# Kernel tuning notes

Hardware: AMD Instinct MI355X
Metric: run time of the kernel (lower is better)

The kernel has to match this reference:

```python
import jax, jax.numpy as jnp
import numpy as np

B, S, D_IN, D_K, D_OUT = 8, 2048, 1024, 64, 64

def setup_inputs() -> dict:
    key = jax.random.key(0)
    k1, k2, k3, k4 = jax.random.split(key, 4)
    sc = 1.0 / np.sqrt(D_IN)
    return {
        "X": jax.random.normal(k1, (B, S, D_IN), dtype=jnp.float32),
        "Wq": jax.random.normal(k2, (D_IN, D_K), dtype=jnp.float32) * sc,
        "Wk": jax.random.normal(k3, (D_IN, D_K), dtype=jnp.float32) * sc,
        "Wv": jax.random.normal(k4, (D_IN, D_OUT), dtype=jnp.float32) * sc,
    }

def reference(X, Wq, Wk, Wv):
    # projections (no bias)
    Q = jnp.einsum('bsd,dk->bsk', X, Wq)   # [B,S,d_k]
    K = jnp.einsum('bsd,dk->bsk', X, Wk)   # [B,S,d_k]
    V = jnp.einsum('bsd,dv->bsv', X, Wv)   # [B,S,d_out]
    d_k = Q.shape[-1]
    S_mat = jnp.einsum('bqk,bsk->bqs', Q, K) / jnp.sqrt(jnp.float32(d_k))
    # causal mask: positions j > i get -inf
    causal = jnp.tril(jnp.ones((X.shape[1], X.shape[1]), dtype=bool))
    S_mat = jnp.where(causal[None, :, :], S_mat, -jnp.inf)
    A = jax.nn.softmax(S_mat, axis=-1)
    return jnp.einsum('bqs,bsv->bqv', A, V)
```

## Files before the change

### kernel.cpp

```cpp
#include <hip/hip_runtime.h>
#include <hip/hip_bf16.h>
#include <cstdint>
#include <cstddef>

#define BATCH 8
#define SEQ   2048
#define DIN   1024

typedef float f32x4 __attribute__((ext_vector_type(4)));
typedef float f32x8 __attribute__((ext_vector_type(8)));
typedef __bf16 bf16x4 __attribute__((ext_vector_type(4)));
typedef __bf16 bf16x8 __attribute__((ext_vector_type(8)));
typedef unsigned short ushort8_t __attribute__((ext_vector_type(8)));

__device__ __forceinline__ unsigned short bfu(float f) {
  __bf16 h = (__bf16)f;
  return __builtin_bit_cast(unsigned short, h);
}

__device__ __forceinline__ bf16x8 cvt8pair(float4 a, float4 b) {
  f32x8 v;
  v[0] = a.x; v[1] = a.y; v[2] = a.z; v[3] = a.w;
  v[4] = b.x; v[5] = b.y; v[6] = b.z; v[7] = b.w;
  return __builtin_convertvector(v, bf16x8);
}

__global__ void pack_w(const float* __restrict__ Wq, const float* __restrict__ Wk,
                       const float* __restrict__ Wv, unsigned short* __restrict__ Wp) {
  const int t = blockIdx.x * blockDim.x + threadIdx.x;
  const int lane = t & 63;
  const int grp = t >> 6;
  const int ks = grp & 31;
  const int nt = grp >> 5;
  const int n = nt * 16 + (lane & 15);
  const int k0 = ks * 32 + ((lane >> 4) << 3);
  const float* W;
  int col;
  float scale = 1.0f;
  if (n < 64)       { W = Wq; col = n;       scale = 0.18033688011112042f; }
  else if (n < 128) { W = Wk; col = n - 64;  }
  else              { W = Wv; col = n - 128; }
  ushort8_t out;
#pragma unroll
  for (int j = 0; j < 8; ++j)
    out[j] = bfu(W[(size_t)(k0 + j) * 64 + col] * scale);
  reinterpret_cast<ushort8_t*>(Wp)[t] = out;
}

__global__ __launch_bounds__(256, 2) void qkv_gemm(
    const float* __restrict__ X, const unsigned short* __restrict__ Wp,
    unsigned short* __restrict__ Qb, unsigned short* __restrict__ Kb,
    unsigned short* __restrict__ Vt) {
  __shared__ ushort8_t Af[2][2048];

  const int tid = threadIdx.x;
  const int lane = tid & 63;
  const int wave = tid >> 6;
  const int l15 = lane & 15;
  const int quad = lane >> 4;
  const int m0 = blockIdx.x * 32;
  const int nt0 = wave * 3;

  const int sr = tid >> 3;
  const int sk = tid & 7;
  const float* xrow = X + (size_t)(m0 + sr) * DIN;

  const ushort8_t* wp = reinterpret_cast<const ushort8_t*>(Wp) + nt0 * 2048 + lane;
  ushort8_t breg[2][3];
#pragma unroll
  for (int p = 0; p < 2; ++p)
#pragma unroll
    for (int nt = 0; nt < 3; ++nt) breg[p][nt] = wp[p * 64 + nt * 2048];

  f32x4 acc[2][3];
#pragma unroll
  for (int mt = 0; mt < 2; ++mt)
#pragma unroll
    for (int nt = 0; nt < 3; ++nt) acc[mt][nt] = (f32x4){0.f, 0.f, 0.f, 0.f};

  auto compute_half = [&](int ksbase, const ushort8_t* A) {
    for (int ksl = 0; ksl < 16; ++ksl) {
      const int ks = ksbase + ksl;
      const int p = ks & 1;
      bf16x8 af0 = __builtin_bit_cast(bf16x8, A[(ksl * 4 + quad) * 32 + l15]);
      bf16x8 af1 = __builtin_bit_cast(bf16x8, A[(ksl * 4 + quad) * 32 + 16 + l15]);
      bf16x8 b0 = __builtin_bit_cast(bf16x8, breg[p][0]);
      bf16x8 b1 = __builtin_bit_cast(bf16x8, breg[p][1]);
      bf16x8 b2 = __builtin_bit_cast(bf16x8, breg[p][2]);
      if (ks < 30) {
#pragma unroll
        for (int nt = 0; nt < 3; ++nt)
          breg[p][nt] = wp[(ks + 2) * 64 + nt * 2048];
      }
      acc[0][0] = __builtin_amdgcn_mfma_f32_16x16x32_bf16(af0, b0, acc[0][0], 0, 0, 0);
      acc[0][1] = __builtin_amdgcn_mfma_f32_16x16x32_bf16(af0, b1, acc[0][1], 0, 0, 0);
      acc[0][2] = __builtin_amdgcn_mfma_f32_16x16x32_bf16(af0, b2, acc[0][2], 0, 0, 0);
      acc[1][0] = __builtin_amdgcn_mfma_f32_16x16x32_bf16(af1, b0, acc[1][0], 0, 0, 0);
      acc[1][1] = __builtin_amdgcn_mfma_f32_16x16x32_bf16(af1, b1, acc[1][1], 0, 0, 0);
      acc[1][2] = __builtin_amdgcn_mfma_f32_16x16x32_bf16(af1, b2, acc[1][2], 0, 0, 0);
    }
  };

  float4 xbuf[16];
#pragma unroll
  for (int p = 0; p < 2; ++p) {
    const float4* src = reinterpret_cast<const float4*>(xrow + (sk + p * 8) * 32);
#pragma unroll
    for (int i = 0; i < 8; ++i) xbuf[p * 8 + i] = src[i];
  }
#pragma unroll
  for (int p = 0; p < 2; ++p) {
    const int ksl = sk + p * 8;
#pragma unroll
    for (int q = 0; q < 4; ++q)
      Af[0][(ksl * 4 + q) * 32 + sr] =
          __builtin_bit_cast(ushort8_t, cvt8pair(xbuf[p * 8 + q * 2], xbuf[p * 8 + q * 2 + 1]));
  }
  __syncthreads();

#pragma unroll
  for (int p = 0; p < 2; ++p) {
    const float4* src = reinterpret_cast<const float4*>(xrow + (16 + sk + p * 8) * 32);
#pragma unroll
    for (int i = 0; i < 8; ++i) xbuf[p * 8 + i] = src[i];
  }

  compute_half(0, Af[0]);

#pragma unroll
  for (int p = 0; p < 2; ++p) {
    const int ksl = sk + p * 8;
#pragma unroll
    for (int q = 0; q < 4; ++q)
      Af[1][(ksl * 4 + q) * 32 + sr] =
          __builtin_bit_cast(ushort8_t, cvt8pair(xbuf[p * 8 + q * 2], xbuf[p * 8 + q * 2 + 1]));
  }
  __syncthreads();

  compute_half(16, Af[1]);

#pragma unroll
  for (int mt = 0; mt < 2; ++mt) {
    const int srow = m0 + mt * 16 + quad * 4;
    const int b = srow >> 11;
    const int s = srow & 2047;
#pragma unroll
    for (int nt = 0; nt < 3; ++nt) {
      const f32x4 a = acc[mt][nt];
      const int n = (nt0 + nt) * 16 + l15;
      if (n < 64) {
#pragma unroll
        for (int r = 0; r < 4; ++r)
          Qb[(size_t)(srow + r) * 64 + n] = bfu(a[r]);
      } else if (n < 128) {
#pragma unroll
        for (int r = 0; r < 4; ++r)
          Kb[(size_t)(srow + r) * 64 + (n - 64)] = bfu(a[r]);
      } else {
        const int dv = n - 128;
        ushort4 t4;
        t4.x = bfu(a[0]); t4.y = bfu(a[1]);
        t4.z = bfu(a[2]); t4.w = bfu(a[3]);
        *reinterpret_cast<ushort4*>(Vt + (((size_t)(b * 64 + dv)) << 11) + s) = t4;
      }
    }
  }
}

__global__ __launch_bounds__(256, 2) void flash_kernel(
    const unsigned short* __restrict__ Qb, const unsigned short* __restrict__ Kb,
    const unsigned short* __restrict__ Vt, float* __restrict__ Out) {
  __shared__ float Olds[4][2][16][68];
  __shared__ float Llds[4][2][16];
  __shared__ __attribute__((aligned(16))) unsigned short Pf[4][2][2][512];

  const int tid = threadIdx.x;
  const int lane = tid & 63;
  const int wave = tid >> 6;
  const int l15 = lane & 15;
  const int quad = lane >> 4;

  const int g = blockIdx.x;
  const int batch = g & 7;
  const int jj = (g >> 3) & 31;
  const int qb = (g < 256) ? (63 - jj) : jj;
  const int q0 = qb * 32;
  const int n64 = (q0 + 95) >> 6;

  bf16x8 qf[2][2];
#pragma unroll
  for (int mt = 0; mt < 2; ++mt) {
    const ushort8_t* qp = reinterpret_cast<const ushort8_t*>(
        Qb + (size_t)(batch * SEQ + q0 + mt * 16 + l15) * 64);
    qf[mt][0] = __builtin_bit_cast(bf16x8, qp[quad]);
    qf[mt][1] = __builtin_bit_cast(bf16x8, qp[4 + quad]);
  }

  const ushort8_t* kbase = reinterpret_cast<const ushort8_t*>(
      Kb + (size_t)(batch * SEQ + l15) * 64);
  const unsigned short* vtb = Vt + ((size_t)(batch * 64) << 11);

  const int pbase = l15 * 8 + (quad >> 1) * 128 + (quad & 1) * 4;

  f32x4 o[2][4];
  float lacc[2];
#pragma unroll
  for (int mt = 0; mt < 2; ++mt) {
    lacc[mt] = 0.f;
#pragma unroll
    for (int i = 0; i < 4; ++i) o[mt][i] = (f32x4){0.f, 0.f, 0.f, 0.f};
  }

  ushort8_t kbuf[8];
  if (wave < n64) {
#pragma unroll
    for (int h = 0; h < 4; ++h) {
      const ushort8_t* kp = kbase + (size_t)(wave * 64 + h * 16) * 8;
      kbuf[h * 2] = kp[quad];
      kbuf[h * 2 + 1] = kp[4 + quad];
    }
  }

  for (int kt = wave; kt < n64; kt += 4) {
    const int k0 = kt * 64;
    f32x4 s[2][4];
#pragma unroll
    for (int h = 0; h < 4; ++h) {
      bf16x8 kf0 = __builtin_bit_cast(bf16x8, kbuf[h * 2]);
      bf16x8 kf1 = __builtin_bit_cast(bf16x8, kbuf[h * 2 + 1]);
#pragma unroll
      for (int mt = 0; mt < 2; ++mt) {
        f32x4 z = (f32x4){0.f, 0.f, 0.f, 0.f};
        z = __builtin_amdgcn_mfma_f32_16x16x32_bf16(kf0, qf[mt][0], z, 0, 0, 0);
        z = __builtin_amdgcn_mfma_f32_16x16x32_bf16(kf1, qf[mt][1], z, 0, 0, 0);
        s[mt][h] = z;
      }
    }
    {
      const int nk = (kt + 4 < n64) ? kt + 4 : n64 - 1;
#pragma unroll
      for (int h = 0; h < 4; ++h) {
        const ushort8_t* kp = kbase + (size_t)(nk * 64 + h * 16) * 8;
        kbuf[h * 2] = kp[quad];
        kbuf[h * 2 + 1] = kp[4 + quad];
      }
    }
    ushort8_t vbuf[8];
#pragma unroll
    for (int c = 0; c < 2; ++c)
#pragma unroll
      for (int nt = 0; nt < 4; ++nt)
        vbuf[c * 4 + nt] = reinterpret_cast<const ushort8_t*>(
            vtb + (((size_t)(nt * 16 + l15)) << 11) + k0 + c * 32)[quad];
    if (kt == n64 - 1) {
#pragma unroll
      for (int mt = 0; mt < 2; ++mt) {
        const int row = q0 + mt * 16 + l15;
#pragma unroll
        for (int h = 0; h < 4; ++h) {
          const int colb = k0 + h * 16 + quad * 4;
#pragma unroll
          for (int r = 0; r < 4; ++r)
            if (colb + r > row) s[mt][h][r] = -INFINITY;
        }
      }
    }
#pragma unroll
    for (int mt = 0; mt < 2; ++mt) {
#pragma unroll
      for (int h = 0; h < 4; ++h) {
        f32x4 p;
#pragma unroll
        for (int r = 0; r < 4; ++r) p[r] = __builtin_amdgcn_exp2f(s[mt][h][r]);
        lacc[mt] += (p[0] + p[1]) + (p[2] + p[3]);
        bf16x4 pk = __builtin_convertvector(p, bf16x4);
        *reinterpret_cast<unsigned long long*>(
            &Pf[wave][mt][h >> 1][pbase + ((h & 1) << 8)]) =
            __builtin_bit_cast(unsigned long long, pk);
      }
    }
#pragma unroll
    for (int c = 0; c < 2; ++c) {
      bf16x8 pfm[2];
#pragma unroll
      for (int mt = 0; mt < 2; ++mt)
        pfm[mt] = __builtin_bit_cast(bf16x8,
            reinterpret_cast<const ushort8_t*>(&Pf[wave][mt][c][0])[lane]);
#pragma unroll
      for (int nt = 0; nt < 4; ++nt) {
        bf16x8 vf = __builtin_bit_cast(bf16x8, vbuf[c * 4 + nt]);
#pragma unroll
        for (int mt = 0; mt < 2; ++mt)
          o[mt][nt] = __builtin_amdgcn_mfma_f32_16x16x32_bf16(pfm[mt], vf, o[mt][nt], 0, 0, 0);
      }
    }
  }

#pragma unroll
  for (int off = 16; off < 64; off <<= 1)
#pragma unroll
    for (int mt = 0; mt < 2; ++mt)
      lacc[mt] += __shfl_xor(lacc[mt], off, 64);

#pragma unroll
  for (int mt = 0; mt < 2; ++mt) {
#pragma unroll
    for (int nt = 0; nt < 4; ++nt)
#pragma unroll
      for (int r = 0; r < 4; ++r)
        Olds[wave][mt][quad * 4 + r][nt * 16 + l15] = o[mt][nt][r];
    if (quad == 0) Llds[wave][mt][l15] = lacc[mt];
  }
  __syncthreads();

  const int col = tid & 63;
  const int r0 = tid >> 6;
#pragma unroll
  for (int row = r0; row < 32; row += 4) {
    const int mt = row >> 4;
    const int rr = row & 15;
    float lstar = 0.f, accv = 0.f;
#pragma unroll
    for (int w = 0; w < 4; ++w) {
      lstar += Llds[w][mt][rr];
      accv += Olds[w][mt][rr][col];
    }
    Out[(size_t)(batch * SEQ + q0 + row) * 64 + col] = accv / lstar;
  }
}

extern "C" void kernel_launch(void* const* d_in, const int* in_sizes, int n_in,
                              void* d_out, int out_size, void* d_ws, size_t ws_size,
                              hipStream_t stream) {
  const float* X  = (const float*)d_in[0];
  const float* Wq = (const float*)d_in[1];
  const float* Wk = (const float*)d_in[2];
  const float* Wv = (const float*)d_in[3];
  float* Out = (float*)d_out;

  char* ws = (char*)d_ws;
  unsigned short* Wp = (unsigned short*)ws;
  unsigned short* Qb = (unsigned short*)(ws + (400 << 10));
  unsigned short* Kb = (unsigned short*)(ws + (400 << 10) + (2 << 20));
  unsigned short* Vt = (unsigned short*)(ws + (400 << 10) + (4 << 20));

  pack_w<<<96, 256, 0, stream>>>(Wq, Wk, Wv, Wp);
  qkv_gemm<<<512, 256, 0, stream>>>(X, Wp, Qb, Kb, Vt);
  flash_kernel<<<512, 256, 0, stream>>>(Qb, Kb, Vt, Out);
}
```

Baseline: 133.5 us.

## Halve flash query tile to 16 rows, double grid, prefetch LDS A fragments

The flash kernel now processes 16 query rows per block instead of 32 and launches 1024 blocks with a four-way interleaved causal ordering, at a launch bound of 4 blocks per CU. The aim is better occupancy and load balance across CUs. It also adds s_setprio around the MFMA sections. In the QKV GEMM, the A fragments are now read from LDS one iteration ahead to hide LDS latency. The trade-off is that K/V tiles are loaded twice as many times overall, since each block covers fewer query rows.

```diff
diff --git a/kernel.cpp b/kernel.cpp
--- a/kernel.cpp
+++ b/kernel.cpp
@@ -79,14 +79,20 @@
     for (int nt = 0; nt < 3; ++nt) acc[mt][nt] = (f32x4){0.f, 0.f, 0.f, 0.f};
 
   auto compute_half = [&](int ksbase, const ushort8_t* A) {
+    ushort8_t a0 = A[quad * 32 + l15];
+    ushort8_t a1 = A[quad * 32 + 16 + l15];
     for (int ksl = 0; ksl < 16; ++ksl) {
       const int ks = ksbase + ksl;
       const int p = ks & 1;
-      bf16x8 af0 = __builtin_bit_cast(bf16x8, A[(ksl * 4 + quad) * 32 + l15]);
-      bf16x8 af1 = __builtin_bit_cast(bf16x8, A[(ksl * 4 + quad) * 32 + 16 + l15]);
+      bf16x8 af0 = __builtin_bit_cast(bf16x8, a0);
+      bf16x8 af1 = __builtin_bit_cast(bf16x8, a1);
       bf16x8 b0 = __builtin_bit_cast(bf16x8, breg[p][0]);
       bf16x8 b1 = __builtin_bit_cast(bf16x8, breg[p][1]);
       bf16x8 b2 = __builtin_bit_cast(bf16x8, breg[p][2]);
+      if (ksl < 15) {
+        a0 = A[((ksl + 1) * 4 + quad) * 32 + l15];
+        a1 = A[((ksl + 1) * 4 + quad) * 32 + 16 + l15];
+      }
       if (ks < 30) {
 #pragma unroll
         for (int nt = 0; nt < 3; ++nt)
@@ -167,12 +173,12 @@
   }
 }
 
-__global__ __launch_bounds__(256, 2) void flash_kernel(
+__global__ __launch_bounds__(256, 4) void flash_kernel(
     const unsigned short* __restrict__ Qb, const unsigned short* __restrict__ Kb,
     const unsigned short* __restrict__ Vt, float* __restrict__ Out) {
-  __shared__ float Olds[4][2][16][68];
-  __shared__ float Llds[4][2][16];
-  __shared__ __attribute__((aligned(16))) unsigned short Pf[4][2][2][512];
+  __shared__ float Olds[4][16][68];
+  __shared__ float Llds[4][16];
+  __shared__ __attribute__((aligned(16))) unsigned short Pf[4][2][512];
 
   const int tid = threadIdx.x;
   const int lane = tid & 63;
@@ -182,18 +188,23 @@
 
   const int g = blockIdx.x;
   const int batch = g & 7;
-  const int jj = (g >> 3) & 31;
-  const int qb = (g < 256) ? (63 - jj) : jj;
-  const int q0 = qb * 32;
-  const int n64 = (q0 + 95) >> 6;
-
-  bf16x8 qf[2][2];
-#pragma unroll
-  for (int mt = 0; mt < 2; ++mt) {
+  const int j = g >> 3;
+  const int jm = j & 31;
+  const int grp = j >> 5;
+  int qb;
+  if (grp == 0)      qb = 127 - jm;
+  else if (grp == 1) qb = jm;
+  else if (grp == 2) qb = 95 - jm;
+  else               qb = 32 + jm;
+  const int q0 = qb * 16;
+  const int n64 = (q0 + 79) >> 6;
+
+  bf16x8 qf[2];
+  {
     const ushort8_t* qp = reinterpret_cast<const ushort8_t*>(
-        Qb + (size_t)(batch * SEQ + q0 + mt * 16 + l15) * 64);
-    qf[mt][0] = __builtin_bit_cast(bf16x8, qp[quad]);
-    qf[mt][1] = __builtin_bit_cast(bf16x8, qp[4 + quad]);
+        Qb + (size_t)(batch * SEQ + q0 + l15) * 64);
+    qf[0] = __builtin_bit_cast(bf16x8, qp[quad]);
+    qf[1] = __builtin_bit_cast(bf16x8, qp[4 + quad]);
   }
 
   const ushort8_t* kbase = reinterpret_cast<const ushort8_t*>(
@@ -202,14 +213,10 @@
 
   const int pbase = l15 * 8 + (quad >> 1) * 128 + (quad & 1) * 4;
 
-  f32x4 o[2][4];
-  float lacc[2];
-#pragma unroll
-  for (int mt = 0; mt < 2; ++mt) {
-    lacc[mt] = 0.f;
-#pragma unroll
-    for (int i = 0; i < 4; ++i) o[mt][i] = (f32x4){0.f, 0.f, 0.f, 0.f};
-  }
+  f32x4 o[4];
+  float lacc = 0.f;
+#pragma unroll
+  for (int i = 0; i < 4; ++i) o[i] = (f32x4){0.f, 0.f, 0.f, 0.f};
 
   ushort8_t kbuf[8];
   if (wave < n64) {
@@ -223,19 +230,18 @@
 
   for (int kt = wave; kt < n64; kt += 4) {
     const int k0 = kt * 64;
-    f32x4 s[2][4];
+    f32x4 s[4];
+    __builtin_amdgcn_s_setprio(1);
 #pragma unroll
     for (int h = 0; h < 4; ++h) {
       bf16x8 kf0 = __builtin_bit_cast(bf16x8, kbuf[h * 2]);
       bf16x8 kf1 = __builtin_bit_cast(bf16x8, kbuf[h * 2 + 1]);
-#pragma unroll
-      for (int mt = 0; mt < 2; ++mt) {
-        f32x4 z = (f32x4){0.f, 0.f, 0.f, 0.f};
-        z = __builtin_amdgcn_mfma_f32_16x16x32_bf16(kf0, qf[mt][0], z, 0, 0, 0);
-        z = __builtin_amdgcn_mfma_f32_16x16x32_bf16(kf1, qf[mt][1], z, 0, 0, 0);
-        s[mt][h] = z;
-      }
-    }
+      f32x4 z = (f32x4){0.f, 0.f, 0.f, 0.f};
+      z = __builtin_amdgcn_mfma_f32_16x16x32_bf16(kf0, qf[0], z, 0, 0, 0);
+      z = __builtin_amdgcn_mfma_f32_16x16x32_bf16(kf1, qf[1], z, 0, 0, 0);
+      s[h] = z;
+    }
+    __builtin_amdgcn_s_setprio(0);
     {
       const int nk = (kt + 4 < n64) ? kt + 4 : n64 - 1;
 #pragma unroll
@@ -253,77 +259,62 @@
         vbuf[c * 4 + nt] = reinterpret_cast<const ushort8_t*>(
             vtb + (((size_t)(nt * 16 + l15)) << 11) + k0 + c * 32)[quad];
     if (kt == n64 - 1) {
-#pragma unroll
-      for (int mt = 0; mt < 2; ++mt) {
-        const int row = q0 + mt * 16 + l15;
-#pragma unroll
-        for (int h = 0; h < 4; ++h) {
-          const int colb = k0 + h * 16 + quad * 4;
-#pragma unroll
-          for (int r = 0; r < 4; ++r)
-            if (colb + r > row) s[mt][h][r] = -INFINITY;
-        }
-      }
-    }
-#pragma unroll
-    for (int mt = 0; mt < 2; ++mt) {
+      const int row = q0 + l15;
 #pragma unroll
       for (int h = 0; h < 4; ++h) {
-        f32x4 p;
-#pragma unroll
-        for (int r = 0; r < 4; ++r) p[r] = __builtin_amdgcn_exp2f(s[mt][h][r]);
-        lacc[mt] += (p[0] + p[1]) + (p[2] + p[3]);
-        bf16x4 pk = __builtin_convertvector(p, bf16x4);
-        *reinterpret_cast<unsigned long long*>(
-            &Pf[wave][mt][h >> 1][pbase + ((h & 1) << 8)]) =
-            __builtin_bit_cast(unsigned long long, pk);
-      }
-    }
+        const int colb = k0 + h * 16 + quad * 4;
+#pragma unroll
+        for (int r = 0; r < 4; ++r)
+          if (colb + r > row) s[h][r] = -INFINITY;
+      }
+    }
+    unsigned long long pk[4];
+#pragma unroll
+    for (int h = 0; h < 4; ++h) {
+      f32x4 p;
+#pragma unroll
+      for (int r = 0; r < 4; ++r) p[r] = __builtin_amdgcn_exp2f(s[h][r]);
+      lacc += (p[0] + p[1]) + (p[2] + p[3]);
+      pk[h] = __builtin_bit_cast(unsigned long long, __builtin_convertvector(p, bf16x4));
+    }
+    *reinterpret_cast<unsigned long long*>(&Pf[wave][0][pbase])       = pk[0];
+    *reinterpret_cast<unsigned long long*>(&Pf[wave][0][pbase + 256]) = pk[1];
+    *reinterpret_cast<unsigned long long*>(&Pf[wave][1][pbase])       = pk[2];
+    *reinterpret_cast<unsigned long long*>(&Pf[wave][1][pbase + 256]) = pk[3];
 #pragma unroll
     for (int c = 0; c < 2; ++c) {
-      bf16x8 pfm[2];
-#pragma unroll
-      for (int mt = 0; mt < 2; ++mt)
-        pfm[mt] = __builtin_bit_cast(bf16x8,
-            reinterpret_cast<const ushort8_t*>(&Pf[wave][mt][c][0])[lane]);
+      bf16x8 pfm = __builtin_bit_cast(bf16x8,
+          reinterpret_cast<const ushort8_t*>(&Pf[wave][c][0])[lane]);
+      __builtin_amdgcn_s_setprio(1);
 #pragma unroll
       for (int nt = 0; nt < 4; ++nt) {
         bf16x8 vf = __builtin_bit_cast(bf16x8, vbuf[c * 4 + nt]);
-#pragma unroll
-        for (int mt = 0; mt < 2; ++mt)
-          o[mt][nt] = __builtin_amdgcn_mfma_f32_16x16x32_bf16(pfm[mt], vf, o[mt][nt], 0, 0, 0);
-      }
-    }
-  }
-
-#pragma unroll
-  for (int off = 16; off < 64; off <<= 1)
-#pragma unroll
-    for (int mt = 0; mt < 2; ++mt)
-      lacc[mt] += __shfl_xor(lacc[mt], off, 64);
-
-#pragma unroll
-  for (int mt = 0; mt < 2; ++mt) {
-#pragma unroll
-    for (int nt = 0; nt < 4; ++nt)
-#pragma unroll
-      for (int r = 0; r < 4; ++r)
-        Olds[wave][mt][quad * 4 + r][nt * 16 + l15] = o[mt][nt][r];
-    if (quad == 0) Llds[wave][mt][l15] = lacc[mt];
-  }
+        o[nt] = __builtin_amdgcn_mfma_f32_16x16x32_bf16(pfm, vf, o[nt], 0, 0, 0);
+      }
+      __builtin_amdgcn_s_setprio(0);
+    }
+  }
+
+  lacc += __shfl_xor(lacc, 16, 64);
+  lacc += __shfl_xor(lacc, 32, 64);
+
+#pragma unroll
+  for (int nt = 0; nt < 4; ++nt)
+#pragma unroll
+    for (int r = 0; r < 4; ++r)
+      Olds[wave][quad * 4 + r][nt * 16 + l15] = o[nt][r];
+  if (quad == 0) Llds[wave][l15] = lacc;
   __syncthreads();
 
   const int col = tid & 63;
   const int r0 = tid >> 6;
 #pragma unroll
-  for (int row = r0; row < 32; row += 4) {
-    const int mt = row >> 4;
-    const int rr = row & 15;
+  for (int row = r0; row < 16; row += 4) {
     float lstar = 0.f, accv = 0.f;
 #pragma unroll
     for (int w = 0; w < 4; ++w) {
-      lstar += Llds[w][mt][rr];
-      accv += Olds[w][mt][rr][col];
+      lstar += Llds[w][row];
+      accv += Olds[w][row][col];
     }
     Out[(size_t)(batch * SEQ + q0 + row) * 64 + col] = accv / lstar;
   }
@@ -346,5 +337,5 @@
 
   pack_w<<<96, 256, 0, stream>>>(Wq, Wk, Wv, Wp);
   qkv_gemm<<<512, 256, 0, stream>>>(X, Wp, Qb, Kb, Vt);
-  flash_kernel<<<512, 256, 0, stream>>>(Qb, Kb, Vt, Out);
-}
+  flash_kernel<<<1024, 256, 0, stream>>>(Qb, Kb, Vt, Out);
+}
```

Measured after the change: 152.7 us. 1.14x slower.

## Store K and V in MFMA fragment order so flash loads are fully coalesced

Applied to the files above, without the earlier changes.

The projection kernel now writes K and V straight into a per-64-key-tile fragment layout that matches the MFMA operand order. Each flash-attention wave can then load its K and V fragments as contiguous 16-byte-per-lane reads, replacing strided row gathers. The change also software-prefetches the next A fragment from LDS in the GEMM loop and raises wave priority around the MFMA sections. The cost is more complex, scattered index math on the GEMM store side.

```diff
diff --git a/kernel.cpp b/kernel.cpp
--- a/kernel.cpp
+++ b/kernel.cpp
@@ -49,8 +49,8 @@
 
 __global__ __launch_bounds__(256, 2) void qkv_gemm(
     const float* __restrict__ X, const unsigned short* __restrict__ Wp,
-    unsigned short* __restrict__ Qb, unsigned short* __restrict__ Kb,
-    unsigned short* __restrict__ Vt) {
+    unsigned short* __restrict__ Qb, unsigned short* __restrict__ Kf,
+    unsigned short* __restrict__ Vf) {
   __shared__ ushort8_t Af[2][2048];
 
   const int tid = threadIdx.x;
@@ -79,14 +79,20 @@
     for (int nt = 0; nt < 3; ++nt) acc[mt][nt] = (f32x4){0.f, 0.f, 0.f, 0.f};
 
   auto compute_half = [&](int ksbase, const ushort8_t* A) {
+    ushort8_t a0 = A[quad * 32 + l15];
+    ushort8_t a1 = A[quad * 32 + 16 + l15];
     for (int ksl = 0; ksl < 16; ++ksl) {
       const int ks = ksbase + ksl;
       const int p = ks & 1;
-      bf16x8 af0 = __builtin_bit_cast(bf16x8, A[(ksl * 4 + quad) * 32 + l15]);
-      bf16x8 af1 = __builtin_bit_cast(bf16x8, A[(ksl * 4 + quad) * 32 + 16 + l15]);
+      bf16x8 af0 = __builtin_bit_cast(bf16x8, a0);
+      bf16x8 af1 = __builtin_bit_cast(bf16x8, a1);
       bf16x8 b0 = __builtin_bit_cast(bf16x8, breg[p][0]);
       bf16x8 b1 = __builtin_bit_cast(bf16x8, breg[p][1]);
       bf16x8 b2 = __builtin_bit_cast(bf16x8, breg[p][2]);
+      if (ksl < 15) {
+        a0 = A[((ksl + 1) * 4 + quad) * 32 + l15];
+        a1 = A[((ksl + 1) * 4 + quad) * 32 + 16 + l15];
+      }
       if (ks < 30) {
 #pragma unroll
         for (int nt = 0; nt < 3; ++nt)
@@ -153,23 +159,30 @@
         for (int r = 0; r < 4; ++r)
           Qb[(size_t)(srow + r) * 64 + n] = bfu(a[r]);
       } else if (n < 128) {
-#pragma unroll
-        for (int r = 0; r < 4; ++r)
-          Kb[(size_t)(srow + r) * 64 + (n - 64)] = bfu(a[r]);
+        const int dk = n - 64;
+        const int dh = dk >> 5, kq = (dk >> 3) & 3, kj = dk & 7;
+        const int kt = s >> 6, hh = (s >> 4) & 3;
+        unsigned short* kdst = Kf + (((size_t)(b * 32 + kt) * 8 + hh * 2 + dh) << 9)
+                                  + (kq * 16 + quad * 4) * 8 + kj;
+#pragma unroll
+        for (int r = 0; r < 4; ++r) kdst[r * 8] = bfu(a[r]);
       } else {
         const int dv = n - 128;
+        const int vnt = dv >> 4, vl = dv & 15;
+        const int kt = s >> 6, vc = (s >> 5) & 1, vq = (s >> 3) & 3, j0 = s & 7;
         ushort4 t4;
         t4.x = bfu(a[0]); t4.y = bfu(a[1]);
         t4.z = bfu(a[2]); t4.w = bfu(a[3]);
-        *reinterpret_cast<ushort4*>(Vt + (((size_t)(b * 64 + dv)) << 11) + s) = t4;
+        *reinterpret_cast<ushort4*>(Vf + (((size_t)(b * 32 + kt) * 8 + vc * 4 + vnt) << 9)
+                                       + (vq * 16 + vl) * 8 + j0) = t4;
       }
     }
   }
 }
 
 __global__ __launch_bounds__(256, 2) void flash_kernel(
-    const unsigned short* __restrict__ Qb, const unsigned short* __restrict__ Kb,
-    const unsigned short* __restrict__ Vt, float* __restrict__ Out) {
+    const unsigned short* __restrict__ Qb, const unsigned short* __restrict__ Kf,
+    const unsigned short* __restrict__ Vf, float* __restrict__ Out) {
   __shared__ float Olds[4][2][16][68];
   __shared__ float Llds[4][2][16];
   __shared__ __attribute__((aligned(16))) unsigned short Pf[4][2][2][512];
@@ -196,9 +209,10 @@
     qf[mt][1] = __builtin_bit_cast(bf16x8, qp[4 + quad]);
   }
 
-  const ushort8_t* kbase = reinterpret_cast<const ushort8_t*>(
-      Kb + (size_t)(batch * SEQ + l15) * 64);
-  const unsigned short* vtb = Vt + ((size_t)(batch * 64) << 11);
+  const ushort8_t* kfb = reinterpret_cast<const ushort8_t*>(Kf)
+                         + (size_t)batch * 32 * 512 + lane;
+  const ushort8_t* vfb = reinterpret_cast<const ushort8_t*>(Vf)
+                         + (size_t)batch * 32 * 512 + lane;
 
   const int pbase = l15 * 8 + (quad >> 1) * 128 + (quad & 1) * 4;
 
@@ -213,17 +227,15 @@
 
   ushort8_t kbuf[8];
   if (wave < n64) {
-#pragma unroll
-    for (int h = 0; h < 4; ++h) {
-      const ushort8_t* kp = kbase + (size_t)(wave * 64 + h * 16) * 8;
-      kbuf[h * 2] = kp[quad];
-      kbuf[h * 2 + 1] = kp[4 + quad];
-    }
+    const ushort8_t* kp = kfb + wave * 512;
+#pragma unroll
+    for (int i = 0; i < 8; ++i) kbuf[i] = kp[i * 64];
   }
 
   for (int kt = wave; kt < n64; kt += 4) {
     const int k0 = kt * 64;
     f32x4 s[2][4];
+    __builtin_amdgcn_s_setprio(1);
 #pragma unroll
     for (int h = 0; h < 4; ++h) {
       bf16x8 kf0 = __builtin_bit_cast(bf16x8, kbuf[h * 2]);
@@ -236,22 +248,19 @@
         s[mt][h] = z;
       }
     }
+    __builtin_amdgcn_s_setprio(0);
     {
       const int nk = (kt + 4 < n64) ? kt + 4 : n64 - 1;
-#pragma unroll
-      for (int h = 0; h < 4; ++h) {
-        const ushort8_t* kp = kbase + (size_t)(nk * 64 + h * 16) * 8;
-        kbuf[h * 2] = kp[quad];
-        kbuf[h * 2 + 1] = kp[4 + quad];
-      }
+      const ushort8_t* kp = kfb + nk * 512;
+#pragma unroll
+      for (int i = 0; i < 8; ++i) kbuf[i] = kp[i * 64];
     }
     ushort8_t vbuf[8];
-#pragma unroll
-    for (int c = 0; c < 2; ++c)
-#pragma unroll
-      for (int nt = 0; nt < 4; ++nt)
-        vbuf[c * 4 + nt] = reinterpret_cast<const ushort8_t*>(
-            vtb + (((size_t)(nt * 16 + l15)) << 11) + k0 + c * 32)[quad];
+    {
+      const ushort8_t* vp = vfb + kt * 512;
+#pragma unroll
+      for (int i = 0; i < 8; ++i) vbuf[i] = vp[i * 64];
+    }
     if (kt == n64 - 1) {
 #pragma unroll
       for (int mt = 0; mt < 2; ++mt) {
@@ -286,6 +295,7 @@
       for (int mt = 0; mt < 2; ++mt)
         pfm[mt] = __builtin_bit_cast(bf16x8,
             reinterpret_cast<const ushort8_t*>(&Pf[wave][mt][c][0])[lane]);
+      __builtin_amdgcn_s_setprio(1);
 #pragma unroll
       for (int nt = 0; nt < 4; ++nt) {
         bf16x8 vf = __builtin_bit_cast(bf16x8, vbuf[c * 4 + nt]);
@@ -293,6 +303,7 @@
         for (int mt = 0; mt < 2; ++mt)
           o[mt][nt] = __builtin_amdgcn_mfma_f32_16x16x32_bf16(pfm[mt], vf, o[mt][nt], 0, 0, 0);
       }
+      __builtin_amdgcn_s_setprio(0);
     }
   }
 
@@ -341,10 +352,10 @@
   char* ws = (char*)d_ws;
   unsigned short* Wp = (unsigned short*)ws;
   unsigned short* Qb = (unsigned short*)(ws + (400 << 10));
-  unsigned short* Kb = (unsigned short*)(ws + (400 << 10) + (2 << 20));
-  unsigned short* Vt = (unsigned short*)(ws + (400 << 10) + (4 << 20));
+  unsigned short* Kf = (unsigned short*)(ws + (400 << 10) + (2 << 20));
+  unsigned short* Vf = (unsigned short*)(ws + (400 << 10) + (4 << 20));
 
   pack_w<<<96, 256, 0, stream>>>(Wq, Wk, Wv, Wp);
-  qkv_gemm<<<512, 256, 0, stream>>>(X, Wp, Qb, Kb, Vt);
-  flash_kernel<<<512, 256, 0, stream>>>(Qb, Kb, Vt, Out);
-}
+  qkv_gemm<<<512, 256, 0, stream>>>(X, Wp, Qb, Kf, Vf);
+  flash_kernel<<<512, 256, 0, stream>>>(Qb, Kf, Vf, Out);
+}
```

Result: faster. 121.1 us, median of 2 (-9.3%).
